# Performance work log

Measured on AMD Instinct MI355X. Metric: run time of the kernel, lower is better.

## Reference

```python
import jax, jax.numpy as jnp
import numpy as np

N = 100000   # nodes
E = 1600000  # edges (avg degree 16)
D = 64       # input_dim = hidden_dim = output_dim
BN_EPS = 1e-5
LEAKY_SLOPE = 0.01


def setup_inputs() -> dict:
    key = jax.random.key(0)
    ks = jax.random.split(key, 8)
    s = 1.0 / np.sqrt(D)
    return {
        "x": jax.random.normal(ks[0], (N, D), jnp.float32),
        "edge_index": jax.random.randint(ks[1], (2, E), 0, N, dtype=jnp.int32),
        "W1": jax.random.uniform(ks[2], (D, D), jnp.float32, -s, s),
        "b1": jnp.zeros((D,), jnp.float32),
        "gamma": jnp.ones((D,), jnp.float32),
        "beta": jnp.zeros((D,), jnp.float32),
        "W2": jax.random.uniform(ks[3], (D, D), jnp.float32, -s, s),
        "b2": jnp.zeros((D,), jnp.float32),
    }


def reference(x, edge_index, W1, b1, gamma, beta, W2, b2):
    n = x.shape[0]
    # GCN: add self-loops, symmetric normalization D^-1/2 (A+I) D^-1/2
    loops = jnp.arange(n, dtype=edge_index.dtype)
    src = jnp.concatenate([edge_index[0], loops])
    dst = jnp.concatenate([edge_index[1], loops])
    deg = jax.ops.segment_sum(jnp.ones_like(dst, dtype=x.dtype), dst, num_segments=n)
    dinv = jnp.where(deg > 0, jax.lax.rsqrt(jnp.maximum(deg, 1.0)), 0.0)
    norm = dinv[src] * dinv[dst]  # [E+N]

    def gcn(h, W, b):
        h = h @ W                              # [N, D]
        msg = h[src] * norm[:, None]           # gather + scale, [E+N, D]
        return jax.ops.segment_sum(msg, dst, num_segments=n) + b

    h = gcn(x, W1, b1)
    # BatchNorm1d (training-mode batch stats, biased variance)
    mu = jnp.mean(h, axis=0)
    var = jnp.mean((h - mu) ** 2, axis=0)
    h = gamma * (h - mu) * jax.lax.rsqrt(var + BN_EPS) + beta
    # LeakyReLU; dropout p=0.0 is identity
    h = jnp.where(h >= 0, h, LEAKY_SLOPE * h)
    return gcn(h, W2, b2)
```

## Files before the change

kernel.cpp:

```cpp
#include <hip/hip_runtime.h>
#include <hip/hip_fp16.h>

#define LEAKY 0.01f
#define BN_EPS 1e-5f
#define NB 512
#define NW 256
#define EMAX 4096
#define BCAP 7168

typedef int v4i __attribute__((ext_vector_type(4)));

__global__ __launch_bounds__(256) void k_pg(const int* __restrict__ src,
                                            const int* __restrict__ dst,
                                            unsigned* __restrict__ barr,
                                            int* __restrict__ bofs,
                                            double* __restrict__ st,
                                            int e, int nper, int n,
                                            const float* __restrict__ X,
                                            const float* __restrict__ W,
                                            __half* __restrict__ Y) {
  __shared__ __align__(16) int smem_i[9216];
  int t = threadIdx.x;
  if (blockIdx.x < NW) {
    int* lcnt = smem_i;
    int* lofs = smem_i + 512;
    int* lcur = smem_i + 1024;
    int* sd   = smem_i + 1536;
    int wb = blockIdx.x;
    if (wb == 0 && t < 128) st[t] = 0.0;
    int S = (e + NW - 1) / NW;
    int s0 = wb * S, s1 = min(e, s0 + S);
    lcnt[t] = 0;
    lcnt[t + 256] = 0;
    lcur[t] = 0;
    lcur[t + 256] = 0;
    __syncthreads();
    for (int i = s0 + t; i < s1; i += 256) atomicAdd(&lcnt[dst[i] / nper], 1);
    __syncthreads();
    int c0 = lcnt[2 * t], c1 = lcnt[2 * t + 1];
    int ts = c0 + c1;
    sd[t] = ts;
    __syncthreads();
    for (int off = 1; off < 256; off <<= 1) {
      int x = (t >= off) ? sd[t - off] : 0;
      __syncthreads();
      sd[t] += x;
      __syncthreads();
    }
    int run = sd[t] - ts;
    lofs[2 * t] = run;
    lofs[2 * t + 1] = run + c0;
    bofs[wb * (NB + 1) + 2 * t] = run;
    bofs[wb * (NB + 1) + 2 * t + 1] = run + c0;
    if (t == 255) bofs[wb * (NB + 1) + NB] = sd[255];
    __syncthreads();
    for (int i = s0 + t; i < s1; i += 256) {
      int d = dst[i];
      int b = d / nper;
      int r = atomicAdd(&lcur[b], 1);
      barr[s0 + lofs[b] + r] = ((unsigned)src[i] << 9) | (unsigned)(d - b * nper);
    }
  } else {
    float(*Ws)[68] = (float(*)[68])smem_i;
    float(*Xs)[68] = (float(*)[68])(smem_i + 4352);
    int rowbase = (blockIdx.x - NW) * 64;
#pragma unroll
    for (int p = 0; p < 4; p++) {
      int idx = (p * 256 + t) * 4;
      *(float4*)&Ws[idx >> 6][idx & 63] = *(const float4*)&W[idx];
      int r = idx >> 6, c = idx & 63;
      int gr = rowbase + r;
      float4 v = (gr < n) ? *(const float4*)&X[(size_t)gr * 64 + c]
                          : make_float4(0.f, 0.f, 0.f, 0.f);
      *(float4*)&Xs[r][c] = v;
    }
    __syncthreads();
    int r = t >> 2;
    int cq = t & 3;
    float acc[16];
#pragma unroll
    for (int j = 0; j < 16; j++) acc[j] = 0.f;
#pragma unroll 4
    for (int k = 0; k < 64; k++) {
      float xv = Xs[r][k];
#pragma unroll
      for (int j = 0; j < 16; j++) acc[j] += xv * Ws[k][cq * 16 + j];
    }
    int gr = rowbase + r;
    if (gr < n) {
      __half2 h2[8];
#pragma unroll
      for (int j = 0; j < 8; j++) h2[j] = __floats2half2_rn(acc[2 * j], acc[2 * j + 1]);
      __half* yp = &Y[(size_t)gr * 64 + cq * 16];
      *(int4*)yp = *(int4*)&h2[0];
      *(int4*)(yp + 8) = *(int4*)&h2[4];
    }
  }
}

__global__ __launch_bounds__(256) void k_csrb(const unsigned* __restrict__ barr,
                                              const int* __restrict__ bofs,
                                              int* __restrict__ csr,
                                              int2* __restrict__ seg2,
                                              float* __restrict__ dinv,
                                              unsigned* __restrict__ Asent,
                                              int n, int nper, int e) {
  __shared__ int eds[EMAX];
  __shared__ int cnt_[256], base_[256], sd[256];
  __shared__ int ssz[256], soff[256], sstart[256];
  int b = blockIdx.x, t = threadIdx.x;
  if (b == 0 && t < 32) Asent[t] = 0u;
  int S = (e + NW - 1) / NW;
  int lo = b * nper;
  int nn = min(nper, n - lo);
  if (nn < 0) nn = 0;
  int st_ = bofs[t * (NB + 1) + b];
  int en_ = bofs[t * (NB + 1) + b + 1];
  int v = en_ - st_;
  sstart[t] = st_;
  ssz[t] = v;
  sd[t] = v;
  __syncthreads();
  for (int off = 1; off < 256; off <<= 1) {
    int x = (t >= off) ? sd[t - off] : 0;
    __syncthreads();
    sd[t] += x;
    __syncthreads();
  }
  soff[t] = sd[t] - v;
  __syncthreads();
  int total = min(sd[255], EMAX);
  int g8 = t >> 3, l8 = t & 7;
  for (int wb = g8; wb < NW; wb += 32) {
    int sz = ssz[wb], of = soff[wb];
    const unsigned* rp = barr + (size_t)wb * S + sstart[wb];
    for (int k = l8; k < sz && of + k < EMAX; k += 8) eds[of + k] = (int)rp[k];
  }
  cnt_[t] = 0;
  __syncthreads();
  for (int i = t; i < total; i += 256) atomicAdd(&cnt_[eds[i] & 511], 1);
  __syncthreads();
  int c = cnt_[t];
  int pc = (t < nn) ? ((c + 15) & ~15) : 0;
  sd[t] = pc;
  __syncthreads();
  for (int off = 1; off < 256; off <<= 1) {
    int x = (t >= off) ? sd[t - off] : 0;
    __syncthreads();
    sd[t] += x;
    __syncthreads();
  }
  base_[t] = sd[t] - pc;
  __syncthreads();
  int bb = b * BCAP;
  if (t < nn) {
    int ba = bb + base_[t];
    seg2[lo + t] = make_int2(ba, ba + pc);
    dinv[lo + t] = rsqrtf((float)(c + 1));
    for (int j = c; j < pc; j++) csr[ba + j] = n;
  }
  __syncthreads();
  cnt_[t] = 0;
  __syncthreads();
  for (int i = t; i < total; i += 256) {
    int vv = eds[i];
    int lcl = vv & 511;
    int r = atomicAdd(&cnt_[lcl], 1);
    csr[bb + base_[lcl] + r] = vv >> 9;
  }
  if (b == 0 && t == 0) dinv[n] = 0.f;
}

__global__ __launch_bounds__(256) void k_gemm2(const __half* __restrict__ Xh,
                                               const float* __restrict__ W,
                                               __half* __restrict__ Y, int n,
                                               const float* __restrict__ dinv,
                                               const double* __restrict__ st,
                                               const float* __restrict__ gamma,
                                               const float* __restrict__ beta) {
  __shared__ float Ws[64][68];
  __shared__ float Xs[64][68];
  __shared__ float smu[64], sisd[64];
  int t = threadIdx.x;
  if (t < 64) {
    double mu = st[t] / n;
    double var = st[64 + t] / n - mu * mu;
    smu[t] = (float)mu;
    sisd[t] = (float)(1.0 / sqrt(var + (double)BN_EPS));
  }
  __syncthreads();
  int rowbase = blockIdx.x * 64;
#pragma unroll
  for (int p = 0; p < 4; p++) {
    int idx = (p * 256 + t) * 4;
    *(float4*)&Ws[idx >> 6][idx & 63] = *(const float4*)&W[idx];
  }
#pragma unroll
  for (int p = 0; p < 2; p++) {
    int idx = (p * 256 + t) * 8;
    int r = idx >> 6, c = idx & 63;
    int gr = rowbase + r;
    float vp[8];
    if (gr < n) {
      int4 hv = *(const int4*)&Xh[(size_t)gr * 64 + c];
      __half2* hp = (__half2*)&hv;
#pragma unroll
      for (int q = 0; q < 4; q++) {
        float2 f = __half22float2(hp[q]);
        vp[2 * q] = f.x;
        vp[2 * q + 1] = f.y;
      }
    } else {
#pragma unroll
      for (int q = 0; q < 8; q++) vp[q] = 0.f;
    }
#pragma unroll
    for (int q = 0; q < 8; q++) {
      float z = gamma[c + q] * (vp[q] - smu[c + q]) * sisd[c + q] + beta[c + q];
      Xs[r][c + q] = (z >= 0.f) ? z : LEAKY * z;
    }
  }
  __syncthreads();
  int r = t >> 2;
  int cq = t & 3;
  float acc[16];
#pragma unroll
  for (int j = 0; j < 16; j++) acc[j] = 0.f;
#pragma unroll 4
  for (int k = 0; k < 64; k++) {
    float xv = Xs[r][k];
#pragma unroll
    for (int j = 0; j < 16; j++) acc[j] += xv * Ws[k][cq * 16 + j];
  }
  int gr = rowbase + r;
  if (gr < n) {
    float dv = dinv[gr];
    __half2 h2[8];
#pragma unroll
    for (int j = 0; j < 8; j++)
      h2[j] = __floats2half2_rn(acc[2 * j] * dv, acc[2 * j + 1] * dv);
    __half* yp = &Y[(size_t)gr * 64 + cq * 16];
    *(int4*)yp = *(int4*)&h2[0];
    *(int4*)(yp + 8) = *(int4*)&h2[4];
  }
}

template <bool WEIGHTED, bool FP16OUT>
__global__ __launch_bounds__(256) void k_agg(const __half* __restrict__ H,
                                             void* __restrict__ Optr,
                                             const int2* __restrict__ seg2,
                                             const int* __restrict__ csr,
                                             const float* __restrict__ dinv,
                                             const float* __restrict__ bias, int n) {
  int wave = (blockIdx.x * 256 + threadIdx.x) >> 6;
  int lane = threadIdx.x & 63;
  int i = wave;
  if (i >= n) return;
  float di = dinv[i];
  int2 sg = seg2[i];
  int s0 = sg.x, s1 = sg.y;
  int m = lane & 31;
  bool loA = lane < 32;
  float2 sf = __half22float2(*(const __half2*)&H[(size_t)i * 64 + 2 * m]);
  float sw = WEIGHTED ? di : 1.f;
  float a0 = loA ? sf.x * sw : 0.f;
  float a1 = loA ? sf.y * sw : 0.f;
  const v4i* cp = (const v4i*)csr;
  int j = s0 >> 2, jend = s1 >> 2;
  v4i q0 = cp[j];
  v4i q1 = cp[j + 1];
  v4i q2 = cp[j + 2];
  v4i q3 = cp[j + 3];
  for (; j < jend; j += 4) {
    v4i p0 = cp[j + 4];
    v4i p1 = cp[j + 5];
    v4i p2 = cp[j + 6];
    v4i p3 = cp[j + 7];
    int i0 = loA ? q0[0] : q0[1];
    int i1 = loA ? q0[2] : q0[3];
    int i2 = loA ? q1[0] : q1[1];
    int i3 = loA ? q1[2] : q1[3];
    int i4 = loA ? q2[0] : q2[1];
    int i5 = loA ? q2[2] : q2[3];
    int i6 = loA ? q3[0] : q3[1];
    int i7 = loA ? q3[2] : q3[3];
    float2 f0 = __half22float2(*(const __half2*)&H[(size_t)i0 * 64 + 2 * m]);
    float2 f1 = __half22float2(*(const __half2*)&H[(size_t)i1 * 64 + 2 * m]);
    float2 f2 = __half22float2(*(const __half2*)&H[(size_t)i2 * 64 + 2 * m]);
    float2 f3 = __half22float2(*(const __half2*)&H[(size_t)i3 * 64 + 2 * m]);
    float2 f4 = __half22float2(*(const __half2*)&H[(size_t)i4 * 64 + 2 * m]);
    float2 f5 = __half22float2(*(const __half2*)&H[(size_t)i5 * 64 + 2 * m]);
    float2 f6 = __half22float2(*(const __half2*)&H[(size_t)i6 * 64 + 2 * m]);
    float2 f7 = __half22float2(*(const __half2*)&H[(size_t)i7 * 64 + 2 * m]);
    if constexpr (WEIGHTED) {
      float w0 = dinv[i0], w1 = dinv[i1], w2 = dinv[i2], w3 = dinv[i3];
      float w4 = dinv[i4], w5 = dinv[i5], w6 = dinv[i6], w7 = dinv[i7];
      a0 += f0.x * w0 + f1.x * w1 + f2.x * w2 + f3.x * w3;
      a1 += f0.y * w0 + f1.y * w1 + f2.y * w2 + f3.y * w3;
      a0 += f4.x * w4 + f5.x * w5 + f6.x * w6 + f7.x * w7;
      a1 += f4.y * w4 + f5.y * w5 + f6.y * w6 + f7.y * w7;
    } else {
      a0 += f0.x + f1.x + f2.x + f3.x;
      a1 += f0.y + f1.y + f2.y + f3.y;
      a0 += f4.x + f5.x + f6.x + f7.x;
      a1 += f4.y + f5.y + f6.y + f7.y;
    }
    q0 = p0;
    q1 = p1;
    q2 = p2;
    q3 = p3;
  }
  a0 += __shfl_xor(a0, 32, 64);
  a1 += __shfl_xor(a1, 32, 64);
  if (loA) {
    float2 bv = *(const float2*)&bias[2 * m];
    float o0 = di * a0 + bv.x;
    float o1 = di * a1 + bv.y;
    if constexpr (FP16OUT) {
      ((__half2*)Optr)[(size_t)i * 32 + m] = __floats2half2_rn(o0, o1);
    } else {
      float2 o;
      o.x = o0;
      o.y = o1;
      *(float2*)&((float*)Optr)[(size_t)i * 64 + 2 * m] = o;
    }
  }
}

__global__ __launch_bounds__(256) void k_bnstats(const __half* __restrict__ H,
                                                 double* __restrict__ st, int n) {
  __shared__ double ds0[8][32], ds1[8][32], dq0[8][32], dq1[8][32];
  int t = threadIdx.x;
  int m = t & 31;
  int g = t >> 5;
  double s0 = 0.0, s1 = 0.0, q0 = 0.0, q1 = 0.0;
  const __half2* H2 = (const __half2*)H;
  for (int r = blockIdx.x * 8 + g; r < n; r += gridDim.x * 8) {
    float2 f = __half22float2(H2[(size_t)r * 32 + m]);
    s0 += f.x;
    s1 += f.y;
    q0 += (double)f.x * f.x;
    q1 += (double)f.y * f.y;
  }
  ds0[g][m] = s0;
  ds1[g][m] = s1;
  dq0[g][m] = q0;
  dq1[g][m] = q1;
  __syncthreads();
  if (g == 0) {
    double a0 = 0, a1 = 0, b0 = 0, b1 = 0;
#pragma unroll
    for (int j = 0; j < 8; j++) {
      a0 += ds0[j][m];
      a1 += ds1[j][m];
      b0 += dq0[j][m];
      b1 += dq1[j][m];
    }
    atomicAdd(&st[2 * m], a0);
    atomicAdd(&st[2 * m + 1], a1);
    atomicAdd(&st[64 + 2 * m], b0);
    atomicAdd(&st[64 + 2 * m + 1], b1);
  }
}

extern "C" void kernel_launch(void* const* d_in, const int* in_sizes, int n_in,
                              void* d_out, int out_size, void* d_ws, size_t ws_size,
                              hipStream_t stream) {
  const float* x     = (const float*)d_in[0];
  const int*   ei    = (const int*)d_in[1];
  const float* W1    = (const float*)d_in[2];
  const float* b1    = (const float*)d_in[3];
  const float* gamma = (const float*)d_in[4];
  const float* beta  = (const float*)d_in[5];
  const float* W2    = (const float*)d_in[6];
  const float* b2    = (const float*)d_in[7];
  float* out = (float*)d_out;

  int n = in_sizes[0] / 64;
  int e = in_sizes[1] / 2;
  const int* srcv = ei;
  const int* dstv = ei + e;
  int nper = (n + NB - 1) / NB;

  char* ws = (char*)d_ws;
  size_t p = 0;
  auto alloc = [&](size_t bytes) {
    void* r = ws + p;
    p += (bytes + 255) & ~(size_t)255;
    return r;
  };
  unsigned* barr = (unsigned*)alloc((size_t)(e + 256) * 4);
  int*      bofs = (int*)alloc((size_t)NW * (NB + 1) * 4);
  int*      csr  = (int*)alloc(((size_t)NB * BCAP + 256) * 4);
  int2*     seg2 = (int2*)alloc((size_t)n * 8);
  float*    dinv = (float*)alloc((size_t)(n + 1) * 4);
  double*   st   = (double*)alloc(128 * 8);
  __half*   A    = (__half*)alloc((size_t)(n + 1) * 64 * 2);
  __half*   B    = (__half*)alloc((size_t)n * 64 * 2);

  int gG = (n + 63) / 64;
  int gAgg = (n + 3) / 4;

  k_pg<<<NW + gG, 256, 0, stream>>>(srcv, dstv, barr, bofs, st, e, nper, n, x, W1, A);
  k_csrb<<<NB, 256, 0, stream>>>(barr, bofs, csr, seg2, dinv,
                                 (unsigned*)(A + (size_t)n * 64), n, nper, e);
  k_agg<true, true><<<gAgg, 256, 0, stream>>>(A, B, seg2, csr, dinv, b1, n);
  k_bnstats<<<256, 256, 0, stream>>>(B, st, n);
  k_gemm2<<<gG, 256, 0, stream>>>(B, W2, A, n, dinv, st, gamma, beta);
  k_agg<false, false><<<gAgg, 256, 0, stream>>>(A, out, seg2, csr, dinv, b2, n);
}
```

Baseline: 184.2 us.

## Prescale layer-1 features by dinv in CSR build and double partition workers

The CSR-build kernel now multiplies each node's fp16 layer-1 features in place by its dinv, after computing it, for the node range it owns. This removes the per-edge dinv gather from the first aggregation, so both aggregations run the same unweighted kernel. The count of partition blocks (NW) also doubles, and each thread in the CSR build now handles two worker slices during the prefix scan. The trade is an extra read-modify-write pass over the feature matrix and one more fp16 rounding step.

```diff
diff --git a/kernel.cpp b/kernel.cpp
--- a/kernel.cpp
+++ b/kernel.cpp
@@ -4,7 +4,7 @@
 #define LEAKY 0.01f
 #define BN_EPS 1e-5f
 #define NB 512
-#define NW 256
+#define NW 512
 #define EMAX 4096
 #define BCAP 7168
 
@@ -103,23 +103,28 @@
                                               int* __restrict__ csr,
                                               int2* __restrict__ seg2,
                                               float* __restrict__ dinv,
-                                              unsigned* __restrict__ Asent,
+                                              __half* __restrict__ A,
                                               int n, int nper, int e) {
   __shared__ int eds[EMAX];
   __shared__ int cnt_[256], base_[256], sd[256];
-  __shared__ int ssz[256], soff[256], sstart[256];
+  __shared__ int ssz[512], soff[512], sstart[512];
   int b = blockIdx.x, t = threadIdx.x;
-  if (b == 0 && t < 32) Asent[t] = 0u;
+  if (b == 0 && t < 32) ((unsigned*)(A + (size_t)n * 64))[t] = 0u;
   int S = (e + NW - 1) / NW;
   int lo = b * nper;
   int nn = min(nper, n - lo);
   if (nn < 0) nn = 0;
-  int st_ = bofs[t * (NB + 1) + b];
-  int en_ = bofs[t * (NB + 1) + b + 1];
-  int v = en_ - st_;
-  sstart[t] = st_;
-  ssz[t] = v;
-  sd[t] = v;
+  int sa0 = bofs[(2 * t) * (NB + 1) + b];
+  int se0 = bofs[(2 * t) * (NB + 1) + b + 1];
+  int sa1 = bofs[(2 * t + 1) * (NB + 1) + b];
+  int se1 = bofs[(2 * t + 1) * (NB + 1) + b + 1];
+  int v0 = se0 - sa0, v1 = se1 - sa1;
+  sstart[2 * t] = sa0;
+  sstart[2 * t + 1] = sa1;
+  ssz[2 * t] = v0;
+  ssz[2 * t + 1] = v1;
+  int ts = v0 + v1;
+  sd[t] = ts;
   __syncthreads();
   for (int off = 1; off < 256; off <<= 1) {
     int x = (t >= off) ? sd[t - off] : 0;
@@ -127,7 +132,9 @@
     sd[t] += x;
     __syncthreads();
   }
-  soff[t] = sd[t] - v;
+  int run = sd[t] - ts;
+  soff[2 * t] = run;
+  soff[2 * t + 1] = run + v0;
   __syncthreads();
   int total = min(sd[255], EMAX);
   int g8 = t >> 3, l8 = t & 7;
@@ -152,12 +159,30 @@
   }
   base_[t] = sd[t] - pc;
   __syncthreads();
+  float* fdv = (float*)sd;
   int bb = b * BCAP;
   if (t < nn) {
     int ba = bb + base_[t];
     seg2[lo + t] = make_int2(ba, ba + pc);
-    dinv[lo + t] = rsqrtf((float)(c + 1));
+    float dv = rsqrtf((float)(c + 1));
+    dinv[lo + t] = dv;
+    fdv[t] = dv;
     for (int j = c; j < pc; j++) csr[ba + j] = n;
+  }
+  __syncthreads();
+  {
+    int4* Ap = (int4*)(A + (size_t)lo * 64);
+    for (int idx = t; idx < nn * 8; idx += 256) {
+      float dv = fdv[idx >> 3];
+      int4 v = Ap[idx];
+      __half2* hp = (__half2*)&v;
+#pragma unroll
+      for (int q = 0; q < 4; q++) {
+        float2 f = __half22float2(hp[q]);
+        hp[q] = __floats2half2_rn(f.x * dv, f.y * dv);
+      }
+      Ap[idx] = v;
+    }
   }
   __syncthreads();
   cnt_[t] = 0;
@@ -245,7 +270,7 @@
   }
 }
 
-template <bool WEIGHTED, bool FP16OUT>
+template <bool FP16OUT>
 __global__ __launch_bounds__(256) void k_agg(const __half* __restrict__ H,
                                              void* __restrict__ Optr,
                                              const int2* __restrict__ seg2,
@@ -262,9 +287,8 @@
   int m = lane & 31;
   bool loA = lane < 32;
   float2 sf = __half22float2(*(const __half2*)&H[(size_t)i * 64 + 2 * m]);
-  float sw = WEIGHTED ? di : 1.f;
-  float a0 = loA ? sf.x * sw : 0.f;
-  float a1 = loA ? sf.y * sw : 0.f;
+  float a0 = loA ? sf.x : 0.f;
+  float a1 = loA ? sf.y : 0.f;
   const v4i* cp = (const v4i*)csr;
   int j = s0 >> 2, jend = s1 >> 2;
   v4i q0 = cp[j];
@@ -292,19 +316,10 @@
     float2 f5 = __half22float2(*(const __half2*)&H[(size_t)i5 * 64 + 2 * m]);
     float2 f6 = __half22float2(*(const __half2*)&H[(size_t)i6 * 64 + 2 * m]);
     float2 f7 = __half22float2(*(const __half2*)&H[(size_t)i7 * 64 + 2 * m]);
-    if constexpr (WEIGHTED) {
-      float w0 = dinv[i0], w1 = dinv[i1], w2 = dinv[i2], w3 = dinv[i3];
-      float w4 = dinv[i4], w5 = dinv[i5], w6 = dinv[i6], w7 = dinv[i7];
-      a0 += f0.x * w0 + f1.x * w1 + f2.x * w2 + f3.x * w3;
-      a1 += f0.y * w0 + f1.y * w1 + f2.y * w2 + f3.y * w3;
-      a0 += f4.x * w4 + f5.x * w5 + f6.x * w6 + f7.x * w7;
-      a1 += f4.y * w4 + f5.y * w5 + f6.y * w6 + f7.y * w7;
-    } else {
-      a0 += f0.x + f1.x + f2.x + f3.x;
-      a1 += f0.y + f1.y + f2.y + f3.y;
-      a0 += f4.x + f5.x + f6.x + f7.x;
-      a1 += f4.y + f5.y + f6.y + f7.y;
-    }
+    a0 += f0.x + f1.x + f2.x + f3.x;
+    a1 += f0.y + f1.y + f2.y + f3.y;
+    a0 += f4.x + f5.x + f6.x + f7.x;
+    a1 += f4.y + f5.y + f6.y + f7.y;
     q0 = p0;
     q1 = p1;
     q2 = p2;
@@ -402,10 +417,9 @@
   int gAgg = (n + 3) / 4;
 
   k_pg<<<NW + gG, 256, 0, stream>>>(srcv, dstv, barr, bofs, st, e, nper, n, x, W1, A);
-  k_csrb<<<NB, 256, 0, stream>>>(barr, bofs, csr, seg2, dinv,
-                                 (unsigned*)(A + (size_t)n * 64), n, nper, e);
-  k_agg<true, true><<<gAgg, 256, 0, stream>>>(A, B, seg2, csr, dinv, b1, n);
+  k_csrb<<<NB, 256, 0, stream>>>(barr, bofs, csr, seg2, dinv, A, n, nper, e);
+  k_agg<true><<<gAgg, 256, 0, stream>>>(A, B, seg2, csr, dinv, b1, n);
   k_bnstats<<<256, 256, 0, stream>>>(B, st, n);
   k_gemm2<<<gG, 256, 0, stream>>>(B, W2, A, n, dinv, st, gamma, beta);
-  k_agg<false, false><<<gAgg, 256, 0, stream>>>(A, out, seg2, csr, dinv, b2, n);
-}
+  k_agg<false><<<gAgg, 256, 0, stream>>>(A, out, seg2, csr, dinv, b2, n);
+}
```

Result: no change. 183.6 us (median of 2 runs) (-0.3%).
